# Kernel tuning notes

Measured on AMD Instinct MI355X. Metric: run time of the kernel, lower is better.

## Reference

```python
import jax, jax.numpy as jnp
import numpy as np
from functools import partial

N = 10000      # nodes
E = 100000     # edges
WIDTH = 64     # node hidden width
KER_W = 1024   # kernel MLP hidden width
KER_IN = 6     # edge feature dim
DEPTH = 6


def setup_inputs() -> dict:
    key = jax.random.key(0)
    ks = jax.random.split(key, 16)

    def glorot(k, shape):
        fan_in = shape[0]
        return jax.random.normal(k, shape, dtype=jnp.float32) / np.sqrt(fan_in)

    inp = {
        "x": jax.random.normal(ks[0], (N, 1), dtype=jnp.float32),
        "edge_index": jax.random.randint(ks[1], (2, E), 0, N, dtype=jnp.int32),
        "edge_attr": jax.random.uniform(ks[2], (E, KER_IN), dtype=jnp.float32),
        # fc1: in_width=1 -> width
        "fc1_w": glorot(ks[3], (1, WIDTH)),
        "fc1_b": jnp.zeros((WIDTH,), jnp.float32),
        # kernel DenseNet: ker_in -> ker_width -> ker_width -> width**2 (ReLU between)
        "k1_w": glorot(ks[4], (KER_IN, KER_W)),
        "k1_b": jnp.zeros((KER_W,), jnp.float32),
        "k2_w": glorot(ks[5], (KER_W, KER_W)),
        "k2_b": jnp.zeros((KER_W,), jnp.float32),
        "k3_w": glorot(ks[6], (KER_W, WIDTH * WIDTH)),
        "k3_b": jnp.zeros((WIDTH * WIDTH,), jnp.float32),
        # NNConv_old root weight + bias
        "root_w": glorot(ks[7], (WIDTH, WIDTH)),
        "conv_b": jnp.zeros((WIDTH,), jnp.float32),
        # fc2: width -> 1
        "fc2_w": glorot(ks[8], (WIDTH, 1)),
        "fc2_b": jnp.zeros((1,), jnp.float32),
    }
    return inp


def reference(x, edge_index, edge_attr, fc1_w, fc1_b, k1_w, k1_b, k2_w, k2_b,
              k3_w, k3_b, root_w, conv_b, fc2_w, fc2_b):
    src = edge_index[0]  # x_j (source, gathered)
    dst = edge_index[1]  # aggregation target

    # Per-edge kernel MLP -> [E, width, width]. edge_attr is constant across
    # depth iterations, so compute the edge weights once (same math).
    h = jax.nn.relu(edge_attr @ k1_w + k1_b)
    h = jax.nn.relu(h @ k2_w + k2_b)
    ew = (h @ k3_w + k3_b).reshape(E, WIDTH, WIDTH)

    # mean aggregation denominators (scatter_mean semantics: deg clamped to 1)
    deg = jax.ops.segment_sum(jnp.ones((E,), jnp.float32), dst, num_segments=N)
    deg = jnp.maximum(deg, 1.0)[:, None]  # [N,1]

    z = x @ fc1_w + fc1_b  # [N, width]
    for _ in range(DEPTH):
        msg = jnp.einsum('ei,eio->eo', z[src], ew)            # gather + per-edge matmul
        agg = jax.ops.segment_sum(msg, dst, num_segments=N)   # scatter-add
        agg = agg / deg                                       # mean
        z = jax.nn.relu(agg + z @ root_w + conv_b)
    return z @ fc2_w + fc2_b  # [N, 1]
```

## Files before the change

### kernel.cpp

```cpp
#include <hip/hip_runtime.h>
#include <hip/hip_bf16.h>

#define N_NODES 10000
#define N_EDGES 100000
#define DEPTH   6
#define E_CHUNK 12500

typedef __attribute__((ext_vector_type(8))) short short8;
typedef __attribute__((ext_vector_type(4))) float f32x4;
typedef unsigned short u16;

__device__ __forceinline__ float bf2f(u16 u) {
    union { float f; unsigned int i; } v; v.i = ((unsigned int)u) << 16; return v.f;
}
__device__ __forceinline__ u16 f2bf(float f) {
    union { float f; unsigned int i; } v; v.f = f;
    unsigned int x = v.i;
    unsigned int r = (x + 0x7fffu + ((x >> 16) & 1u)) >> 16;
    return (u16)r;
}

__device__ __forceinline__ void gload_lds16(const void* g, void* s) {
    __builtin_amdgcn_global_load_lds((const __attribute__((address_space(1))) void*)g,
                                     (__attribute__((address_space(3))) void*)s, 16, 0, 0);
}

__global__ void k2_transpose_kernel(const float* __restrict__ k2w, u16* __restrict__ k2T) {
    int idx = blockIdx.x * 256 + threadIdx.x;
    int n = idx >> 10, k = idx & 1023;
    k2T[idx] = f2bf(k2w[k * 1024 + n]);
}
__global__ void k3_permT_kernel(const float* __restrict__ k3w, u16* __restrict__ k3pT) {
    int idx = blockIdx.x * 256 + threadIdx.x;
    int n = idx >> 10, c = idx & 1023;
    k3pT[idx] = f2bf(k3w[(size_t)c * 4096 + (n & 63) * 64 + (n >> 6)]);
}
__global__ void b3_permute_kernel(const float* __restrict__ b3, float* __restrict__ b3p) {
    int n = blockIdx.x * 256 + threadIdx.x;
    if (n >= 4096) return;
    b3p[n] = b3[(n & 63) * 64 + (n >> 6)];
}

__global__ void deg_kernel(const int* __restrict__ ei, float* __restrict__ deg) {
    int e = blockIdx.x * 256 + threadIdx.x;
    if (e < N_EDGES) atomicAdd(&deg[ei[N_EDGES + e]], 1.0f);
}

__global__ void gemm1_kernel(const float* __restrict__ ea, const float* __restrict__ k1w,
                             const float* __restrict__ k1b, u16* __restrict__ h1, int e0) {
    int idx = blockIdx.x * 256 + threadIdx.x;
    int c = idx & 1023;
    int e = (idx >> 10) + e0;
    float acc = k1b[c];
#pragma unroll
    for (int i = 0; i < 6; i++) acc += ea[e * 6 + i] * k1w[i * 1024 + c];
    h1[idx] = f2bf(fmaxf(acc, 0.0f));
}

template <int NOUT, bool RELU>
__global__ __launch_bounds__(256) void gemm128_kernel(const u16* __restrict__ A,
                                                      const u16* __restrict__ BT,
                                                      const float* __restrict__ bias,
                                                      u16* __restrict__ C, int M) {
    constexpr int K = 1024;
    __shared__ __align__(16) u16 Alds[128 * 32];
    __shared__ __align__(16) u16 Blds[128 * 32];

    const int t = threadIdx.x;
    const int lane = t & 63, w = t >> 6;
    const int wm = w >> 1, wn = w & 1;
    const int fm = lane & 15, q = lane >> 4;
    const int m0 = blockIdx.y * 128;
    const int n0 = blockIdx.x * 128;

    f32x4 acc[4][4];
#pragma unroll
    for (int a = 0; a < 4; a++)
#pragma unroll
        for (int b = 0; b < 4; b++) acc[a][b] = (f32x4){0.f, 0.f, 0.f, 0.f};

    int ar0 = m0 + (t >> 2);        if (ar0 >= M) ar0 = M - 1;
    int ar1 = m0 + 64 + (t >> 2);   if (ar1 >= M) ar1 = M - 1;
    const u16* gA0 = A + (size_t)ar0 * K + (t & 3) * 8;
    const u16* gA1 = A + (size_t)ar1 * K + (t & 3) * 8;
    const u16* gB0 = BT + (size_t)(n0 + (t >> 2)) * K + (t & 3) * 8;
    const u16* gB1 = BT + (size_t)(n0 + 64 + (t >> 2)) * K + (t & 3) * 8;
    u16* lA0 = &Alds[t * 8];
    u16* lA1 = &Alds[2048 + t * 8];
    u16* lB0 = &Blds[t * 8];
    u16* lB1 = &Blds[2048 + t * 8];

    for (int k0 = 0; k0 < K; k0 += 32) {
        gload_lds16(gA0 + k0, lA0);
        gload_lds16(gA1 + k0, lA1);
        gload_lds16(gB0 + k0, lB0);
        gload_lds16(gB1 + k0, lB1);
        __syncthreads();
        short8 af[4], bf[4];
#pragma unroll
        for (int mi = 0; mi < 4; mi++)
            af[mi] = *reinterpret_cast<const short8*>(&Alds[(wm * 64 + mi * 16 + fm) * 32 + q * 8]);
#pragma unroll
        for (int ni = 0; ni < 4; ni++)
            bf[ni] = *reinterpret_cast<const short8*>(&Blds[(wn * 64 + ni * 16 + fm) * 32 + q * 8]);
#pragma unroll
        for (int mi = 0; mi < 4; mi++)
#pragma unroll
            for (int ni = 0; ni < 4; ni++)
                acc[mi][ni] = __builtin_amdgcn_mfma_f32_16x16x32_bf16(af[mi], bf[ni], acc[mi][ni], 0, 0, 0);
        __syncthreads();
    }

#pragma unroll
    for (int mi = 0; mi < 4; mi++) {
#pragma unroll
        for (int ni = 0; ni < 4; ni++) {
            int col = n0 + wn * 64 + ni * 16 + fm;
            float bsv = bias[col];
#pragma unroll
            for (int r = 0; r < 4; r++) {
                int row = m0 + wm * 64 + mi * 16 + q * 4 + r;
                if (row < M) {
                    float v = acc[mi][ni][r] + bsv;
                    if (RELU) v = fmaxf(v, 0.0f);
                    C[(size_t)row * NOUT + col] = f2bf(v);
                }
            }
        }
    }
}

__global__ __launch_bounds__(256, 2) void gemm_msg_kernel(
    const u16* __restrict__ A, const u16* __restrict__ BT,
    const float* __restrict__ bias, const int* __restrict__ ei,
    const float* __restrict__ z, float* __restrict__ agg, int M) {
    constexpr int K = 1024;
    __shared__ __align__(16) u16 Alds[128 * 32];
    __shared__ __align__(16) u16 Blds[256 * 32];

    const int t = threadIdx.x;
    const int lane = t & 63, w = t >> 6;
    const int wm = w >> 1, wn = w & 1;
    const int fm = lane & 15, q = lane >> 4;
    const int m0 = blockIdx.y * 128;
    const int n0 = blockIdx.x * 256;

    f32x4 acc[4][8];
#pragma unroll
    for (int a = 0; a < 4; a++)
#pragma unroll
        for (int b = 0; b < 8; b++) acc[a][b] = (f32x4){0.f, 0.f, 0.f, 0.f};

    int ar0 = m0 + (t >> 2);        if (ar0 >= M) ar0 = M - 1;
    int ar1 = m0 + 64 + (t >> 2);   if (ar1 >= M) ar1 = M - 1;
    const u16* gA0 = A + (size_t)ar0 * K + (t & 3) * 8;
    const u16* gA1 = A + (size_t)ar1 * K + (t & 3) * 8;
    const u16* gB0 = BT + (size_t)(n0 + (t >> 2)) * K + (t & 3) * 8;
    const u16* gB1 = BT + (size_t)(n0 + 64 + (t >> 2)) * K + (t & 3) * 8;
    const u16* gB2 = BT + (size_t)(n0 + 128 + (t >> 2)) * K + (t & 3) * 8;
    const u16* gB3 = BT + (size_t)(n0 + 192 + (t >> 2)) * K + (t & 3) * 8;
    u16* lA0 = &Alds[t * 8];
    u16* lA1 = &Alds[2048 + t * 8];
    u16* lB0 = &Blds[t * 8];
    u16* lB1 = &Blds[2048 + t * 8];
    u16* lB2 = &Blds[4096 + t * 8];
    u16* lB3 = &Blds[6144 + t * 8];

    for (int k0 = 0; k0 < K; k0 += 32) {
        gload_lds16(gA0 + k0, lA0);
        gload_lds16(gA1 + k0, lA1);
        gload_lds16(gB0 + k0, lB0);
        gload_lds16(gB1 + k0, lB1);
        gload_lds16(gB2 + k0, lB2);
        gload_lds16(gB3 + k0, lB3);
        __syncthreads();
        short8 af[4], bf[8];
#pragma unroll
        for (int mi = 0; mi < 4; mi++)
            af[mi] = *reinterpret_cast<const short8*>(&Alds[(wm * 64 + mi * 16 + fm) * 32 + q * 8]);
#pragma unroll
        for (int ni = 0; ni < 8; ni++)
            bf[ni] = *reinterpret_cast<const short8*>(&Blds[(wn * 128 + ni * 16 + fm) * 32 + q * 8]);
#pragma unroll
        for (int mi = 0; mi < 4; mi++)
#pragma unroll
            for (int ni = 0; ni < 8; ni++)
                acc[mi][ni] = __builtin_amdgcn_mfma_f32_16x16x32_bf16(af[mi], bf[ni], acc[mi][ni], 0, 0, 0);
        __syncthreads();
    }

    const int o0 = blockIdx.x * 4 + wn * 2;
    float bsv[8];
#pragma unroll
    for (int ni = 0; ni < 8; ni++)
        bsv[ni] = bias[n0 + wn * 128 + ni * 16 + fm];
#pragma unroll
    for (int mi = 0; mi < 4; mi++) {
#pragma unroll
        for (int r = 0; r < 4; r++) {
            int e = m0 + wm * 64 + mi * 16 + q * 4 + r;
            float p0 = 0.f, p1 = 0.f;
            int dst = 0;
            if (e < M) {
                int src = ei[e];
                dst = ei[N_EDGES + e];
                const float* zs = z + (size_t)src * 64;
                float zv[4];
#pragma unroll
                for (int j = 0; j < 4; j++) zv[j] = zs[j * 16 + fm];
#pragma unroll
                for (int ni = 0; ni < 4; ni++) {
                    p0 += (acc[mi][ni][r] + bsv[ni]) * zv[ni];
                    p1 += (acc[mi][ni + 4][r] + bsv[ni + 4]) * zv[ni];
                }
            }
            p0 += __shfl_xor(p0, 1);  p1 += __shfl_xor(p1, 1);
            p0 += __shfl_xor(p0, 2);  p1 += __shfl_xor(p1, 2);
            p0 += __shfl_xor(p0, 4);  p1 += __shfl_xor(p1, 4);
            p0 += __shfl_xor(p0, 8);  p1 += __shfl_xor(p1, 8);
            if (fm == 0 && e < M) {
                atomicAdd(&agg[(size_t)dst * 64 + o0], p0);
                atomicAdd(&agg[(size_t)dst * 64 + o0 + 1], p1);
            }
        }
    }
}

__global__ void z0_kernel(const float* __restrict__ x, const float* __restrict__ w,
                          const float* __restrict__ b, float* __restrict__ z) {
    int idx = blockIdx.x * 256 + threadIdx.x;
    int n = idx >> 6, o = idx & 63;
    z[idx] = x[n] * w[o] + b[o];
}

__global__ __launch_bounds__(256) void update_kernel(const float* __restrict__ zin,
                                                     const float* __restrict__ agg,
                                                     const float* __restrict__ deg,
                                                     const float* __restrict__ rootw,
                                                     const float* __restrict__ convb,
                                                     float* __restrict__ zout) {
    int n = blockIdx.x * 4 + (threadIdx.x >> 6);
    int o = threadIdx.x & 63;
    float r = convb[o];
    const float* zr = zin + (size_t)n * 64;
#pragma unroll 8
    for (int i = 0; i < 64; i++) r += zr[i] * rootw[i * 64 + o];
    float d = deg[n];
    d = d < 1.0f ? 1.0f : d;
    float v = agg[(size_t)n * 64 + o] / d + r;
    zout[(size_t)n * 64 + o] = fmaxf(v, 0.0f);
}

__global__ void final_kernel(const float* __restrict__ z, const float* __restrict__ w,
                             const float* __restrict__ b, float* __restrict__ out) {
    int n = blockIdx.x * 256 + threadIdx.x;
    if (n >= N_NODES) return;
    float acc = b[0];
#pragma unroll 8
    for (int o = 0; o < 64; o++) acc += z[(size_t)n * 64 + o] * w[o];
    out[n] = acc;
}

__global__ void dbg_kernel(float* __restrict__ out, float val, int n) {
    int i = blockIdx.x * 256 + threadIdx.x;
    if (i < n) out[i] = val;
}

extern "C" void kernel_launch(void* const* d_in, const int* in_sizes, int n_in,
                              void* d_out, int out_size, void* d_ws, size_t ws_size,
                              hipStream_t stream) {
    const float* x     = (const float*)d_in[0];
    const int*   ei    = (const int*)  d_in[1];
    const float* ea    = (const float*)d_in[2];
    const float* fc1w  = (const float*)d_in[3];
    const float* fc1b  = (const float*)d_in[4];
    const float* k1w   = (const float*)d_in[5];
    const float* k1b   = (const float*)d_in[6];
    const float* k2w   = (const float*)d_in[7];
    const float* k2b   = (const float*)d_in[8];
    const float* k3w   = (const float*)d_in[9];
    const float* k3b   = (const float*)d_in[10];
    const float* rootw = (const float*)d_in[11];
    const float* convb = (const float*)d_in[12];
    const float* fc2w  = (const float*)d_in[13];
    const float* fc2b  = (const float*)d_in[14];
    float* out = (float*)d_out;

    const size_t NEED = 249000000;
    if (ws_size < NEED) {
        dbg_kernel<<<(N_NODES + 255) / 256, 256, 0, stream>>>(out, (float)(ws_size >> 20), N_NODES);
        return;
    }

    char* p = (char*)d_ws;
    auto alloc = [&](size_t bytes) {
        char* r = p;
        p += (bytes + 255) & ~(size_t)255;
        return r;
    };
    u16*   h2   = (u16*)  alloc((size_t)N_EDGES * 1024 * 2);
    u16*   h1ch = (u16*)  alloc((size_t)E_CHUNK * 1024 * 2);
    u16*   k2T  = (u16*)  alloc((size_t)1024 * 1024 * 2);
    u16*   k3pT = (u16*)  alloc((size_t)4096 * 1024 * 2);
    float* b3p  = (float*)alloc(4096 * 4);
    float* zA   = (float*)alloc((size_t)N_NODES * 64 * 4);
    float* zB   = (float*)alloc((size_t)N_NODES * 64 * 4);
    float* agg  = (float*)alloc((size_t)N_NODES * 64 * 4);
    float* deg  = (float*)alloc((size_t)N_NODES * 4);

    hipMemsetAsync(deg, 0, (size_t)N_NODES * 4, stream);

    k2_transpose_kernel<<<(1024 * 1024) / 256, 256, 0, stream>>>(k2w, k2T);
    k3_permT_kernel<<<(4096 * 1024) / 256, 256, 0, stream>>>(k3w, k3pT);
    b3_permute_kernel<<<16, 256, 0, stream>>>(k3b, b3p);
    deg_kernel<<<(N_EDGES + 255) / 256, 256, 0, stream>>>(ei, deg);

    for (int e0 = 0; e0 < N_EDGES; e0 += E_CHUNK) {
        gemm1_kernel<<<(E_CHUNK * 1024) / 256, 256, 0, stream>>>(ea, k1w, k1b, h1ch, e0);
        dim3 g2(1024 / 128, (E_CHUNK + 127) / 128);
        gemm128_kernel<1024, true><<<g2, 256, 0, stream>>>(
            h1ch, k2T, k2b, h2 + (size_t)e0 * 1024, E_CHUNK);
    }

    z0_kernel<<<(N_NODES * 64) / 256, 256, 0, stream>>>(x, fc1w, fc1b, zA);

    float* zin = zA;
    float* zout = zB;
    for (int d = 0; d < DEPTH; d++) {
        hipMemsetAsync(agg, 0, (size_t)N_NODES * 64 * 4, stream);
        dim3 g3(4096 / 256, (N_EDGES + 127) / 128);
        gemm_msg_kernel<<<g3, 256, 0, stream>>>(h2, k3pT, b3p, ei, zin, agg, N_EDGES);
        update_kernel<<<N_NODES / 4, 256, 0, stream>>>(zin, agg, deg, rootw, convb, zout);
        float* tmp = zin; zin = zout; zout = tmp;
    }

    final_kernel<<<(N_NODES + 255) / 256, 256, 0, stream>>>(zin, fc2w, fc2b, out);
}
```

Before: 7.679 ms.

## Double-buffer LDS tiles in fused edge-weight GEMM message kernel

Doubles the A and B shared-memory tiles in gemm_msg_kernel and prefetches the next K-slice into the alternate buffer while MFMAs run on the current one. This drops one of the two block barriers per K step and is meant to hide global-to-LDS load latency behind compute. The kernel now needs twice the LDS, and the minimum-two-blocks occupancy hint is removed. Together these may lower occupancy or let register usage grow.

```diff
diff --git a/kernel.cpp b/kernel.cpp
--- a/kernel.cpp
+++ b/kernel.cpp
@@ -130,13 +130,13 @@
     }
 }
 
-__global__ __launch_bounds__(256, 2) void gemm_msg_kernel(
+__global__ __launch_bounds__(256) void gemm_msg_kernel(
     const u16* __restrict__ A, const u16* __restrict__ BT,
     const float* __restrict__ bias, const int* __restrict__ ei,
     const float* __restrict__ z, float* __restrict__ agg, int M) {
     constexpr int K = 1024;
-    __shared__ __align__(16) u16 Alds[128 * 32];
-    __shared__ __align__(16) u16 Blds[256 * 32];
+    __shared__ __align__(16) u16 Alds[2 * 128 * 32];
+    __shared__ __align__(16) u16 Blds[2 * 256 * 32];
 
     const int t = threadIdx.x;
     const int lane = t & 63, w = t >> 6;
@@ -166,27 +166,38 @@
     u16* lB2 = &Blds[4096 + t * 8];
     u16* lB3 = &Blds[6144 + t * 8];
 
+    auto stage = [&](int k0, int buf) {
+        int ao = buf * 4096, bo = buf * 8192;
+        gload_lds16(gA0 + k0, lA0 + ao);
+        gload_lds16(gA1 + k0, lA1 + ao);
+        gload_lds16(gB0 + k0, lB0 + bo);
+        gload_lds16(gB1 + k0, lB1 + bo);
+        gload_lds16(gB2 + k0, lB2 + bo);
+        gload_lds16(gB3 + k0, lB3 + bo);
+    };
+
+    stage(0, 0);
+    int cur = 0;
     for (int k0 = 0; k0 < K; k0 += 32) {
-        gload_lds16(gA0 + k0, lA0);
-        gload_lds16(gA1 + k0, lA1);
-        gload_lds16(gB0 + k0, lB0);
-        gload_lds16(gB1 + k0, lB1);
-        gload_lds16(gB2 + k0, lB2);
-        gload_lds16(gB3 + k0, lB3);
         __syncthreads();
+        if (k0 + 32 < K) stage(k0 + 32, cur ^ 1);
+
+        const int aoff = cur * 4096, boff = cur * 8192;
         short8 af[4], bf[8];
 #pragma unroll
         for (int mi = 0; mi < 4; mi++)
-            af[mi] = *reinterpret_cast<const short8*>(&Alds[(wm * 64 + mi * 16 + fm) * 32 + q * 8]);
+            af[mi] = *reinterpret_cast<const short8*>(
+                &Alds[aoff + (wm * 64 + mi * 16 + fm) * 32 + q * 8]);
 #pragma unroll
         for (int ni = 0; ni < 8; ni++)
-            bf[ni] = *reinterpret_cast<const short8*>(&Blds[(wn * 128 + ni * 16 + fm) * 32 + q * 8]);
+            bf[ni] = *reinterpret_cast<const short8*>(
+                &Blds[boff + (wn * 128 + ni * 16 + fm) * 32 + q * 8]);
 #pragma unroll
         for (int mi = 0; mi < 4; mi++)
 #pragma unroll
             for (int ni = 0; ni < 8; ni++)
                 acc[mi][ni] = __builtin_amdgcn_mfma_f32_16x16x32_bf16(af[mi], bf[ni], acc[mi][ni], 0, 0, 0);
-        __syncthreads();
+        cur ^= 1;
     }
 
     const int o0 = blockIdx.x * 4 + wn * 2;
```

Result: no change. 7.707 ms (+0.4%).
